# Optimization experiments

Measured on AMD Instinct MI355X. Metric: run time of the kernel, lower is better.

The kernel has to match this reference:

```python
import jax, jax.numpy as jnp
import numpy as np

NEG_INF = -9e15  # matches torch code's -9000000000000000.0
ALPHA = 0.1      # LeakyReLU negative slope


def setup_inputs() -> dict:
    key = jax.random.key(0)
    k1, k2, k3, k4 = jax.random.split(key, 4)
    N, D = 4096, 2048
    input_features = jax.random.normal(k1, (N, D), dtype=jnp.float32)
    adj_mat = jax.random.normal(k2, (N, N), dtype=jnp.float32)
    # parameters of GraphAttentionLayer(2048, 2048)
    W = jax.random.normal(k3, (D, D), dtype=jnp.float32) * 0.02
    a = jax.random.normal(k4, (2 * D, 1), dtype=jnp.float32) * 0.02
    return {"input_features": input_features, "adj_mat": adj_mat, "W": W, "a": a}


def reference(input_features, adj_mat, W, a):
    x = input_features  # [N, D]
    D = W.shape[1]
    # --- GNN.forward: cosine similarity adjacency ---
    dot = x @ x.T                                  # [N, N]
    lens = jnp.sqrt(jnp.sum(x * x, axis=1))        # [N]
    cos_sim = dot / (lens[:, None] * lens[None, :])
    new_adj = adj_mat * cos_sim                    # [N, N]
    # --- GraphAttentionLayer.forward ---
    h = x @ W                                      # [N, D]
    # concat trick: e_ij = leakyrelu(a1.h_i + a2.h_j), avoiding O(N^2*2D) tensor
    a1, a2 = a[:D, 0], a[D:, 0]
    s1 = h @ a1                                    # [N]
    s2 = h @ a2                                    # [N]
    e = jax.nn.leaky_relu(s1[:, None] + s2[None, :], ALPHA)  # [N, N]
    att_logits = jnp.where(new_adj > 0, e, NEG_INF)
    attention = jax.nn.softmax(att_logits, axis=1)  # dropout is identity at eval
    h_prime = attention @ h                        # [N, D]
    return jax.nn.elu(h_prime)                     # concat=True -> elu
```

## Files before the change

kernel.cpp:

```cpp
#include <hip/hip_runtime.h>
#include <hip/hip_bf16.h>
#include <cmath>

typedef unsigned short u16;
typedef unsigned char u8;
typedef unsigned int u32;
typedef __attribute__((ext_vector_type(8))) _Float16 f16x8;
typedef __attribute__((ext_vector_type(4))) float f32x4;

__device__ __forceinline__ float bf2f(u16 v) {
    union { u32 u; float f; } c; c.u = (u32)v << 16; return c.f;
}
__device__ __forceinline__ u16 f2bf(float f) {
    union { float f; u32 u; } c; c.f = f;
    u32 u = c.u;
    u += 0x7FFF + ((u >> 16) & 1);
    return (u16)(u >> 16);
}
__device__ __forceinline__ u16 f2h(float f) {
    _Float16 h = (_Float16)f; u16 r; __builtin_memcpy(&r, &h, 2); return r;
}
__device__ __forceinline__ float h2f(u16 b) {
    _Float16 h; __builtin_memcpy(&h, &b, 2); return (float)h;
}

__device__ __forceinline__ void gld_lds16(const void* g, void* l) {
    __builtin_amdgcn_global_load_lds(
        (const __attribute__((address_space(1))) void*)g,
        (__attribute__((address_space(3))) void*)l, 16, 0, 0);
}

__global__ __launch_bounds__(256) void sniff_kernel(const u16* __restrict__ x,
                                                    u32* __restrict__ flag) {
    const int t = threadIdx.x;
    int local = 0;
    for (int i = t; i < 4096; i += 256) {
        const int e = (x[i] >> 7) & 0xFF;
        if (e >= 110 && e <= 137) local++;
    }
#pragma unroll
    for (int o = 32; o > 0; o >>= 1) local += __shfl_down(local, o, 64);
    __shared__ int s[4];
    if ((t & 63) == 0) s[t >> 6] = local;
    __syncthreads();
    if (t == 0) {
        const int tot = s[0] + s[1] + s[2] + s[3];
        *flag = (tot >= 3200) ? 1u : 0u;
    }
}

__global__ __launch_bounds__(256) void prep_kernel(
    const void* __restrict__ xin, const void* __restrict__ Win,
    const void* __restrict__ ain,
    u16* __restrict__ xhi, u16* __restrict__ xlo,
    u16* __restrict__ WT, u16* __restrict__ aout,
    const u32* __restrict__ flag, int N, int D)
{
    __shared__ u16 tile[64][68];
    const bool isbf = (*flag != 0);
    const int b = blockIdx.x;
    const int t = threadIdx.x;

    if (b < 1024) {
        const long base = (long)b * 8192;
#pragma unroll
        for (int it = 0; it < 8; ++it) {
            const long i = base + (long)(it * 256 + t) * 4;
            float v[4];
            if (isbf) {
                ushort4 u = *(const ushort4*)((const u16*)xin + i);
                v[0] = bf2f(u.x); v[1] = bf2f(u.y); v[2] = bf2f(u.z); v[3] = bf2f(u.w);
            } else {
                float4 f = *(const float4*)((const float*)xin + i);
                v[0] = f.x; v[1] = f.y; v[2] = f.z; v[3] = f.w;
            }
            ushort4 hi, lo;
            u16* hp = &hi.x; u16* lp = &lo.x;
#pragma unroll
            for (int k = 0; k < 4; ++k) {
                _Float16 h = (_Float16)v[k];
                u16 hb; __builtin_memcpy(&hb, &h, 2);
                hp[k] = hb;
                lp[k] = f2h(v[k] - (float)h);
            }
            *(ushort4*)(xhi + i) = hi;
            *(ushort4*)(xlo + i) = lo;
        }
    } else if (b < 2048) {
        const int tt = b - 1024;
        const int bc = (tt & 31) * 64;
        const int br = (tt >> 5) * 64;
        const int lr = t >> 4;
        const int lc = (t & 15) * 4;
#pragma unroll
        for (int s = 0; s < 4; ++s) {
            const int r = lr + s * 16;
            float v[4];
            if (isbf) {
                ushort4 u = *(const ushort4*)((const u16*)Win + (size_t)(br + r) * D + bc + lc);
                v[0] = bf2f(u.x); v[1] = bf2f(u.y); v[2] = bf2f(u.z); v[3] = bf2f(u.w);
            } else {
                float4 f = *(const float4*)((const float*)Win + (size_t)(br + r) * D + bc + lc);
                v[0] = f.x; v[1] = f.y; v[2] = f.z; v[3] = f.w;
            }
            tile[r][lc + 0] = f2h(v[0]); tile[r][lc + 1] = f2h(v[1]);
            tile[r][lc + 2] = f2h(v[2]); tile[r][lc + 3] = f2h(v[3]);
        }
        __syncthreads();
#pragma unroll
        for (int s = 0; s < 4; ++s) {
            const int oc = lr + s * 16;
            ushort4 v;
            v.x = tile[lc + 0][oc]; v.y = tile[lc + 1][oc];
            v.z = tile[lc + 2][oc]; v.w = tile[lc + 3][oc];
            *(ushort4*)&WT[(size_t)(bc + oc) * D + br + lc] = v;
        }
    } else {
        for (int i = t; i < 2 * D; i += 256) {
            float v = isbf ? bf2f(((const u16*)ain)[i]) : ((const float*)ain)[i];
            aout[i] = f2h(v);
        }
    }
}

#define NMASK 528
#define MAXFIX 1024
#define MTAU 0.125f
__global__ __launch_bounds__(256, 2) void fused_mask_h(
    const u16* __restrict__ Xhi, const u16* __restrict__ Xlo, int ldx,
    u16* __restrict__ P, int N,
    const void* __restrict__ adj,
    const u16* __restrict__ WT, int D,
    u16* __restrict__ h,
    const u32* __restrict__ dflag)
{
    __shared__ alignas(16) u16 sm[2][128 * 64];

    const int tid = threadIdx.x;
    const int wave = tid >> 6, lane = tid & 63;
    const int wr = wave >> 1, wc = wave & 1;
    const int q = lane >> 4, mrow = lane & 15;
    const int srow8 = lane >> 3;
    const int gslot = (lane & 7) ^ srow8;

    const int bid = blockIdx.x;
    const bool isbf = (*dflag != 0);

    if (bid < NMASK) {
        const int idx = bid;
        int bm = (int)((__builtin_sqrtf(8.0f * idx + 1.0f) - 1.0f) * 0.5f);
        while ((bm + 1) * (bm + 2) / 2 <= idx) ++bm;
        while (bm * (bm + 1) / 2 > idx) --bm;
        const int bn = idx - bm * (bm + 1) / 2;

        const u16* Ab = Xhi + (size_t)bm * 128 * ldx;
        const u16* Bb = Xhi + (size_t)bn * 128 * ldx;

        f32x4 acc[4][4] = {};

        const int T = ldx >> 6;
        for (int t = 0; t < T; ++t) {
            const int kt = t * 64;
#pragma unroll
            for (int it = 0; it < 4; ++it) {
                const int c = wave * 4 + it;
                const int row = c * 8 + srow8;
                const size_t go = (size_t)row * ldx + kt + gslot * 8;
                gld_lds16(Ab + go, &sm[0][c * 512]);
                gld_lds16(Bb + go, &sm[1][c * 512]);
            }
            __syncthreads();

            f16x8 a[2][4], b[2][4];
#pragma unroll
            for (int ks = 0; ks < 2; ++ks)
#pragma unroll
                for (int i = 0; i < 4; ++i) {
                    const int ra = wr * 64 + i * 16 + mrow;
                    const int rb = wc * 64 + i * 16 + mrow;
                    const int sa = ((q + 4 * ks) ^ (mrow & 7)) * 8;
                    a[ks][i] = *(const f16x8*)&sm[0][ra * 64 + sa];
                    b[ks][i] = *(const f16x8*)&sm[1][rb * 64 + sa];
                }
#pragma unroll
            for (int i = 0; i < 4; ++i)
#pragma unroll
                for (int j = 0; j < 4; ++j) {
                    acc[i][j] = __builtin_amdgcn_mfma_f32_16x16x32_f16(
                        a[0][i], b[0][j], acc[i][j], 0, 0, 0);
                    acc[i][j] = __builtin_amdgcn_mfma_f32_16x16x32_f16(
                        a[1][i], b[1][j], acc[i][j], 0, 0, 0);
                }
            __syncthreads();
        }

        const u16* adjB = (const u16*)adj;
        const float* adjF = (const float*)adj;
        const float tau = isbf ? -1.0f : MTAU;

        u8* sgn = (u8*)sm;
        u32* list = (u32*)((u8*)sm + 24576);
        int* cntp = (int*)((u8*)sm + 28672);

        if (tid == 0) *cntp = 0;
#pragma unroll
        for (int i = 0; i < 4; ++i)
#pragma unroll
            for (int j = 0; j < 4; ++j)
#pragma unroll
                for (int r = 0; r < 4; ++r) {
                    const int rl = wr * 64 + i * 16 + q * 4 + r;
                    const int cl = wc * 64 + j * 16 + mrow;
                    const float v = acc[i][j][r];
                    sgn[rl * 132 + cl] = v > 0.f ? (u8)1
                                       : (v < 0.f ? (u8)2 : (u8)0);
                }
        __syncthreads();

#pragma unroll
        for (int i = 0; i < 4; ++i)
#pragma unroll
            for (int j = 0; j < 4; ++j)
#pragma unroll
                for (int r = 0; r < 4; ++r)
                    if (__builtin_fabsf(acc[i][j][r]) < tau) {
                        const int rl = wr * 64 + i * 16 + q * 4 + r;
                        const int cl = wc * 64 + j * 16 + mrow;
                        const int ix = atomicAdd(cntp, 1);
                        if (ix < MAXFIX) list[ix] = (u32)((rl << 8) | cl);
                    }
        __syncthreads();

        const int nfix = (*cntp < MAXFIX) ? *cntp : MAXFIX;
        for (int e = wave; e < nfix; e += 4) {
            const u32 pk = list[e];
            const int rl = (int)(pk >> 8), cl = (int)(pk & 255u);
            const u16* arh = Xhi + (size_t)(bm * 128 + rl) * ldx;
            const u16* arl = Xlo + (size_t)(bm * 128 + rl) * ldx;
            const u16* brh = Xhi + (size_t)(bn * 128 + cl) * ldx;
            const u16* brl = Xlo + (size_t)(bn * 128 + cl) * ldx;
            float ssum = 0.f;
#pragma unroll
            for (int kk = 0; kk < 4; ++kk) {
                const int k = kk * 512 + lane * 8;
                const f16x8 vah = *(const f16x8*)&arh[k];
                const f16x8 val2 = *(const f16x8*)&arl[k];
                const f16x8 vbh = *(const f16x8*)&brh[k];
                const f16x8 vbl = *(const f16x8*)&brl[k];
#pragma unroll
                for (int u = 0; u < 8; ++u)
                    ssum += ((float)vah[u] + (float)val2[u]) *
                            ((float)vbh[u] + (float)vbl[u]);
            }
#pragma unroll
            for (int o = 32; o > 0; o >>= 1) ssum += __shfl_xor(ssum, o, 64);
            if (lane == 0)
                sgn[rl * 132 + cl] = ssum > 0.f ? (u8)1
                                   : (ssum < 0.f ? (u8)2 : (u8)0);
        }
        __syncthreads();

        {
            const int c = tid & 127;
            const int r0 = tid >> 7;
#pragma unroll 4
            for (int s = 0; s < 64; ++s) {
                const int rr = r0 + 2 * s;
                const u8 s3 = sgn[rr * 132 + c];
                const size_t aidx = (size_t)(bm * 128 + rr) * N + bn * 128 + c;
                const float av = isbf ? bf2f(adjB[aidx]) : adjF[aidx];
                const bool f = (s3 == 1) ? (av > 0.f)
                             : (s3 == 2) ? (av < 0.f) : false;
                P[aidx] = f ? (u16)1 : (u16)0;
            }
        }

        if (bm != bn) {
            const int bl_ = tid & 63;
            const int a0 = tid >> 6;
#pragma unroll 4
            for (int s = 0; s < 32; ++s) {
                const int a = a0 + 4 * s;
#pragma unroll
                for (int hb = 0; hb < 2; ++hb) {
                    const int b = bl_ + 64 * hb;
                    const u8 s3 = sgn[b * 132 + a];
                    const size_t aidx = (size_t)(bn * 128 + a) * N + bm * 128 + b;
                    const float av = isbf ? bf2f(adjB[aidx]) : adjF[aidx];
                    const bool f = (s3 == 1) ? (av > 0.f)
                                 : (s3 == 2) ? (av < 0.f) : false;
                    P[aidx] = f ? (u16)1 : (u16)0;
                }
            }
        }
    } else {
        const int j = bid - NMASK;
        const int bn = j & 15;
        const int bm = j >> 4;

        const u16* Ab = Xhi + (size_t)bm * 128 * ldx;
        const u16* Bb = WT + (size_t)bn * 128 * D;

        f32x4 acc[4][4] = {};

        const int T = D >> 6;
        for (int t = 0; t < T; ++t) {
            const int kt = t * 64;
#pragma unroll
            for (int it = 0; it < 4; ++it) {
                const int c = wave * 4 + it;
                const int row = c * 8 + srow8;
                gld_lds16(Ab + (size_t)row * ldx + kt + gslot * 8,
                          &sm[0][c * 512]);
                gld_lds16(Bb + (size_t)row * D + kt + gslot * 8,
                          &sm[1][c * 512]);
            }
            __syncthreads();

            f16x8 a[2][4], b[2][4];
#pragma unroll
            for (int ks = 0; ks < 2; ++ks)
#pragma unroll
                for (int i = 0; i < 4; ++i) {
                    const int ra = wr * 64 + i * 16 + mrow;
                    const int rb = wc * 64 + i * 16 + mrow;
                    const int sa = ((q + 4 * ks) ^ (mrow & 7)) * 8;
                    a[ks][i] = *(const f16x8*)&sm[0][ra * 64 + sa];
                    b[ks][i] = *(const f16x8*)&sm[1][rb * 64 + sa];
                }
#pragma unroll
            for (int i = 0; i < 4; ++i)
#pragma unroll
                for (int jj = 0; jj < 4; ++jj) {
                    acc[i][jj] = __builtin_amdgcn_mfma_f32_16x16x32_f16(
                        a[0][i], b[0][jj], acc[i][jj], 0, 0, 0);
                    acc[i][jj] = __builtin_amdgcn_mfma_f32_16x16x32_f16(
                        a[1][i], b[1][jj], acc[i][jj], 0, 0, 0);
                }
            __syncthreads();
        }

        const int row0 = bm * 128 + wr * 64 + q * 4;
        const int col0 = bn * 128 + wc * 64 + mrow;
#pragma unroll
        for (int i = 0; i < 4; ++i)
#pragma unroll
            for (int jj = 0; jj < 4; ++jj)
#pragma unroll
                for (int r = 0; r < 4; ++r)
                    h[(size_t)(row0 + i * 16 + r) * D + col0 + jj * 16] =
                        f2h(acc[i][jj][r]);
    }
}

__global__ __launch_bounds__(256) void post1_kernel(
    const u16* __restrict__ h, const u16* __restrict__ a,
    float* __restrict__ s1, float* __restrict__ s2,
    u16* __restrict__ hT, int N, int D)
{
    __shared__ u16 tile[64][68];
    __shared__ float r1[4], r2[4];
    const int b = blockIdx.x;
    const int t = threadIdx.x;

    if (b < N) {
        const u16* hr = h + (size_t)b * D;
        const int k0 = t * 8;
        float acc1 = 0.f, acc2 = 0.f;
#pragma unroll
        for (int u = 0; u < 8; u += 4) {
            ushort4 hv  = *(const ushort4*)&hr[k0 + u];
            ushort4 a1v = *(const ushort4*)&a[k0 + u];
            ushort4 a2v = *(const ushort4*)&a[D + k0 + u];
            acc1 += h2f(hv.x) * h2f(a1v.x) + h2f(hv.y) * h2f(a1v.y)
                  + h2f(hv.z) * h2f(a1v.z) + h2f(hv.w) * h2f(a1v.w);
            acc2 += h2f(hv.x) * h2f(a2v.x) + h2f(hv.y) * h2f(a2v.y)
                  + h2f(hv.z) * h2f(a2v.z) + h2f(hv.w) * h2f(a2v.w);
        }
        const int lane = t & 63, wv = t >> 6;
#pragma unroll
        for (int o = 32; o > 0; o >>= 1) {
            acc1 += __shfl_down(acc1, o, 64);
            acc2 += __shfl_down(acc2, o, 64);
        }
        if (lane == 0) { r1[wv] = acc1; r2[wv] = acc2; }
        __syncthreads();
        if (t == 0) {
            s1[b] = r1[0] + r1[1] + r1[2] + r1[3];
            s2[b] = r2[0] + r2[1] + r2[2] + r2[3];
        }
    } else {
        const int tt = b - N;
        const int bc = (tt & 31) * 64;
        const int br = (tt >> 5) * 64;
        const int lr = t >> 4;
        const int lc = (t & 15) * 4;
#pragma unroll
        for (int s = 0; s < 4; ++s) {
            const int r = lr + s * 16;
            ushort4 v = *(const ushort4*)&h[(size_t)(br + r) * D + bc + lc];
            tile[r][lc + 0] = v.x; tile[r][lc + 1] = v.y;
            tile[r][lc + 2] = v.z; tile[r][lc + 3] = v.w;
        }
        __syncthreads();
#pragma unroll
        for (int s = 0; s < 4; ++s) {
            const int oc = lr + s * 16;
            ushort4 v;
            v.x = tile[lc + 0][oc]; v.y = tile[lc + 1][oc];
            v.z = tile[lc + 2][oc]; v.w = tile[lc + 3][oc];
            *(ushort4*)&hT[(size_t)(bc + oc) * N + br + lc] = v;
        }
    }
}

__global__ __launch_bounds__(256) void softmax_kernel(
    u16* __restrict__ P, const float* __restrict__ s1,
    const float* __restrict__ s2, int N)
{
    const int row = blockIdx.x;
    const int t = threadIdx.x;
    const int lane = t & 63, wv = t >> 6;
    u16* prow = P + (size_t)row * N;
    const float s1v = s1[row];

    float e[16];
#pragma unroll
    for (int it = 0; it < 16; ++it) {
        const int j = it * 256 + t;
        const u16 f = prow[j];
        float ev = s1v + s2[j];
        ev = ev >= 0.f ? ev : 0.1f * ev;
        e[it] = f ? ev : -9.0e15f;
    }
    float m = -3.4e38f;
#pragma unroll
    for (int it = 0; it < 16; ++it) m = fmaxf(m, e[it]);
#pragma unroll
    for (int o = 32; o > 0; o >>= 1) m = fmaxf(m, __shfl_xor(m, o, 64));
    __shared__ float red[8];
    if (lane == 0) red[wv] = m;
    __syncthreads();
    m = fmaxf(fmaxf(red[0], red[1]), fmaxf(red[2], red[3]));

    float sum = 0.f;
#pragma unroll
    for (int it = 0; it < 16; ++it) {
        e[it] = expf(fminf(e[it] - m, 0.0f));
        sum += e[it];
    }
#pragma unroll
    for (int o = 32; o > 0; o >>= 1) sum += __shfl_xor(sum, o, 64);
    if (lane == 0) red[4 + wv] = sum;
    __syncthreads();
    sum = red[4] + red[5] + red[6] + red[7];
    const float inv = 1.f / fmaxf(sum, 1e-30f);
#pragma unroll
    for (int it = 0; it < 16; ++it) {
        const int j = it * 256 + t;
        prow[j] = f2h(e[it] * inv);
    }
}

__global__ __launch_bounds__(256, 2) void gemm_elu(
    const u16* __restrict__ A, int lda,
    const u16* __restrict__ B, int ldb,
    u16* __restrict__ C, int ldc,
    int K, const u32* __restrict__ dflag)
{
    __shared__ alignas(16) u16 sm[2][128 * 64];

    const int tid = threadIdx.x;
    const int wave = tid >> 6, lane = tid & 63;
    const int wr = wave >> 1, wc = wave & 1;
    const int q = lane >> 4, mrow = lane & 15;
    const int srow8 = lane >> 3;
    const int gslot = (lane & 7) ^ srow8;

    const int bm = blockIdx.y;
    const int bn = blockIdx.x;

    const u16* Ab = A + (size_t)bm * 128 * lda;
    const u16* Bb = B + (size_t)bn * 128 * ldb;

    f32x4 acc[4][4] = {};

    const int T = K >> 6;
    for (int t = 0; t < T; ++t) {
        const int kt = t * 64;
#pragma unroll
        for (int it = 0; it < 4; ++it) {
            const int c = wave * 4 + it;
            const int row = c * 8 + srow8;
            gld_lds16(Ab + (size_t)row * lda + kt + gslot * 8, &sm[0][c * 512]);
            gld_lds16(Bb + (size_t)row * ldb + kt + gslot * 8, &sm[1][c * 512]);
        }
        __syncthreads();

        f16x8 a[2][4], b[2][4];
#pragma unroll
        for (int ks = 0; ks < 2; ++ks)
#pragma unroll
            for (int i = 0; i < 4; ++i) {
                const int ra = wr * 64 + i * 16 + mrow;
                const int rb = wc * 64 + i * 16 + mrow;
                const int sa = ((q + 4 * ks) ^ (mrow & 7)) * 8;
                a[ks][i] = *(const f16x8*)&sm[0][ra * 64 + sa];
                b[ks][i] = *(const f16x8*)&sm[1][rb * 64 + sa];
            }
#pragma unroll
        for (int i = 0; i < 4; ++i)
#pragma unroll
            for (int j = 0; j < 4; ++j) {
                acc[i][j] = __builtin_amdgcn_mfma_f32_16x16x32_f16(
                    a[0][i], b[0][j], acc[i][j], 0, 0, 0);
                acc[i][j] = __builtin_amdgcn_mfma_f32_16x16x32_f16(
                    a[1][i], b[1][j], acc[i][j], 0, 0, 0);
            }
        __syncthreads();
    }

    const bool isbf = (*dflag != 0);
    float* outF = (float*)C;
    const int row0 = bm * 128 + wr * 64 + q * 4;
    const int col0 = bn * 128 + wc * 64 + mrow;
#pragma unroll
    for (int i = 0; i < 4; ++i)
#pragma unroll
        for (int j = 0; j < 4; ++j)
#pragma unroll
            for (int r = 0; r < 4; ++r) {
                const int row = row0 + i * 16 + r;
                const int col = col0 + j * 16;
                const float v = acc[i][j][r];
                const float o = v > 0.0f ? v : expm1f(v);
                if (isbf) C[(size_t)row * ldc + col] = f2bf(o);
                else      outF[(size_t)row * ldc + col] = o;
            }
}

extern "C" void kernel_launch(void* const* d_in, const int* in_sizes, int n_in,
                              void* d_out, int out_size, void* d_ws, size_t ws_size,
                              hipStream_t stream)
{
    const void* x   = d_in[0];
    const void* adj = d_in[1];
    const void* W   = d_in[2];
    const void* a   = d_in[3];

    const int N = 4096, D = 2048;

    u16* xhi = (u16*)d_ws;
    u16* xlo = xhi + (size_t)N * D;
    u16* WT  = xlo + (size_t)N * D;
    u16* h   = WT  + (size_t)D * D;
    u16* P   = h   + (size_t)N * D;
    u16* af  = P   + (size_t)N * N;
    float* s1 = (float*)(af + 4096);
    float* s2 = s1 + N;
    u32* flag = (u32*)(s2 + N);

    sniff_kernel<<<1, 256, 0, stream>>>((const u16*)x, flag);
    prep_kernel<<<dim3(2049), 256, 0, stream>>>(x, W, a, xhi, xlo, WT, af,
                                                flag, N, D);
    fused_mask_h<<<dim3(1040), 256, 0, stream>>>(
        xhi, xlo, D, P, N, adj, WT, D, h, flag);
    post1_kernel<<<dim3(N + 2048), 256, 0, stream>>>(h, af, s1, s2, xlo, N, D);
    softmax_kernel<<<dim3(N), 256, 0, stream>>>(P, s1, s2, N);
    gemm_elu<<<dim3(D / 128, N / 128), 256, 0, stream>>>(
        P, N, xlo, N, (u16*)d_out, D, N, flag);
}
```

Baseline: 428.1 us.

## Precompute 2-bit adjacency sign map in prep kernel and vectorize mask writes

Adds 1024 blocks to the prep kernel that read the full adjacency matrix once, coalesced, and pack each element's sign into 2 bits. The mask epilogue in fused_mask_h then reads this compact map instead of strided fp32/bf16 adjacency values, and writes P as ushort4 vectors. The aim is to remove uncoalesced, transposed adjacency reads from the GEMM-tile epilogue. The cost is an extra full pass over adj plus a small sign buffer, and the 4-way byte gathers from sgn in the transposed path may cause LDS bank conflicts.

```diff
diff --git a/kernel.cpp b/kernel.cpp
--- a/kernel.cpp
+++ b/kernel.cpp
@@ -51,9 +51,10 @@
 
 __global__ __launch_bounds__(256) void prep_kernel(
     const void* __restrict__ xin, const void* __restrict__ Win,
-    const void* __restrict__ ain,
+    const void* __restrict__ ain, const void* __restrict__ adjin,
     u16* __restrict__ xhi, u16* __restrict__ xlo,
     u16* __restrict__ WT, u16* __restrict__ aout,
+    u8* __restrict__ asgn,
     const u32* __restrict__ flag, int N, int D)
 {
     __shared__ u16 tile[64][68];
@@ -115,10 +116,53 @@
             v.z = tile[lc + 2][oc]; v.w = tile[lc + 3][oc];
             *(ushort4*)&WT[(size_t)(bc + oc) * D + br + lc] = v;
         }
-    } else {
+    } else if (b == 2048) {
         for (int i = t; i < 2 * D; i += 256) {
             float v = isbf ? bf2f(((const u16*)ain)[i]) : ((const float*)ain)[i];
             aout[i] = f2h(v);
+        }
+    } else {
+        const long base = (long)(b - 2049) * 16384;
+#pragma unroll
+        for (int it = 0; it < 4; ++it) {
+            const long e0 = base + (long)(it * 256 + t) * 16;
+            u8 bytes[4];
+            if (isbf) {
+                const u16* ap = (const u16*)adjin + e0;
+#pragma unroll
+                for (int j = 0; j < 4; ++j) {
+                    ushort4 v = *(const ushort4*)(ap + j * 4);
+                    const u16 vv[4] = {v.x, v.y, v.z, v.w};
+                    u8 bb = 0;
+#pragma unroll
+                    for (int k = 0; k < 4; ++k) {
+                        const u16 m = (u16)(vv[k] & 0x7FFF);
+                        const u8 c = (m == 0) ? (u8)0
+                                   : ((vv[k] >> 15) ? (u8)2 : (u8)1);
+                        bb |= (u8)(c << (2 * k));
+                    }
+                    bytes[j] = bb;
+                }
+            } else {
+                const u32* ap = (const u32*)adjin + e0;
+#pragma unroll
+                for (int j = 0; j < 4; ++j) {
+                    uint4 v = *(const uint4*)(ap + j * 4);
+                    const u32 vv[4] = {v.x, v.y, v.z, v.w};
+                    u8 bb = 0;
+#pragma unroll
+                    for (int k = 0; k < 4; ++k) {
+                        const u32 m = vv[k] & 0x7FFFFFFFu;
+                        const u8 c = (m == 0) ? (u8)0
+                                   : ((vv[k] >> 31) ? (u8)2 : (u8)1);
+                        bb |= (u8)(c << (2 * k));
+                    }
+                    bytes[j] = bb;
+                }
+            }
+            uchar4 ov;
+            ov.x = bytes[0]; ov.y = bytes[1]; ov.z = bytes[2]; ov.w = bytes[3];
+            *(uchar4*)(asgn + (e0 >> 2)) = ov;
         }
     }
 }
@@ -129,7 +173,7 @@
 __global__ __launch_bounds__(256, 2) void fused_mask_h(
     const u16* __restrict__ Xhi, const u16* __restrict__ Xlo, int ldx,
     u16* __restrict__ P, int N,
-    const void* __restrict__ adj,
+    const u8* __restrict__ asgn,
     const u16* __restrict__ WT, int D,
     u16* __restrict__ h,
     const u32* __restrict__ dflag)
@@ -144,7 +188,6 @@
     const int gslot = (lane & 7) ^ srow8;
 
     const int bid = blockIdx.x;
-    const bool isbf = (*dflag != 0);
 
     if (bid < NMASK) {
         const int idx = bid;
@@ -194,8 +237,7 @@
             __syncthreads();
         }
 
-        const u16* adjB = (const u16*)adj;
-        const float* adjF = (const float*)adj;
+        const bool isbf = (*dflag != 0);
         const float tau = isbf ? -1.0f : MTAU;
 
         u8* sgn = (u8*)sm;
@@ -261,36 +303,39 @@
         __syncthreads();
 
         {
-            const int c = tid & 127;
-            const int r0 = tid >> 7;
-#pragma unroll 4
-            for (int s = 0; s < 64; ++s) {
-                const int rr = r0 + 2 * s;
-                const u8 s3 = sgn[rr * 132 + c];
-                const size_t aidx = (size_t)(bm * 128 + rr) * N + bn * 128 + c;
-                const float av = isbf ? bf2f(adjB[aidx]) : adjF[aidx];
-                const bool f = (s3 == 1) ? (av > 0.f)
-                             : (s3 == 2) ? (av < 0.f) : false;
-                P[aidx] = f ? (u16)1 : (u16)0;
+            const int c0 = (tid & 31) * 4;
+            const int r0 = tid >> 5;
+#pragma unroll
+            for (int s = 0; s < 16; ++s) {
+                const int rr = r0 + 8 * s;
+                const size_t aidx = (size_t)(bm * 128 + rr) * N + bn * 128 + c0;
+                const u8 ab = asgn[aidx >> 2];
+                const u32 sw = *(const u32*)&sgn[rr * 132 + c0];
+                ushort4 ov;
+                ov.x = ((sw         & 0xFF) & (u32)(ab        & 3)) ? (u16)1 : (u16)0;
+                ov.y = (((sw >>  8) & 0xFF) & (u32)((ab >> 2) & 3)) ? (u16)1 : (u16)0;
+                ov.z = (((sw >> 16) & 0xFF) & (u32)((ab >> 4) & 3)) ? (u16)1 : (u16)0;
+                ov.w = (((sw >> 24) & 0xFF) & (u32)((ab >> 6) & 3)) ? (u16)1 : (u16)0;
+                *(ushort4*)&P[aidx] = ov;
             }
         }
 
         if (bm != bn) {
-            const int bl_ = tid & 63;
-            const int a0 = tid >> 6;
-#pragma unroll 4
-            for (int s = 0; s < 32; ++s) {
-                const int a = a0 + 4 * s;
-#pragma unroll
-                for (int hb = 0; hb < 2; ++hb) {
-                    const int b = bl_ + 64 * hb;
-                    const u8 s3 = sgn[b * 132 + a];
-                    const size_t aidx = (size_t)(bn * 128 + a) * N + bm * 128 + b;
-                    const float av = isbf ? bf2f(adjB[aidx]) : adjF[aidx];
-                    const bool f = (s3 == 1) ? (av > 0.f)
-                                 : (s3 == 2) ? (av < 0.f) : false;
-                    P[aidx] = f ? (u16)1 : (u16)0;
-                }
+            const int b0 = (tid & 31) * 4;
+            const int a0 = tid >> 5;
+#pragma unroll
+            for (int s = 0; s < 16; ++s) {
+                const int a = a0 + 8 * s;
+                const size_t aidx = (size_t)(bn * 128 + a) * N + bm * 128 + b0;
+                const u8 ab = asgn[aidx >> 2];
+                ushort4 ov;
+                u16* op = &ov.x;
+#pragma unroll
+                for (int j = 0; j < 4; ++j) {
+                    const u8 s3 = sgn[(b0 + j) * 132 + a];
+                    op[j] = (u16)((s3 & ((ab >> (2 * j)) & 3)) ? 1 : 0);
+                }
+                *(ushort4*)&P[aidx] = ov;
             }
         }
     } else {
@@ -559,12 +604,13 @@
     float* s1 = (float*)(af + 4096);
     float* s2 = s1 + N;
     u32* flag = (u32*)(s2 + N);
+    u8* asgn = (u8*)(flag + 16);
 
     sniff_kernel<<<1, 256, 0, stream>>>((const u16*)x, flag);
-    prep_kernel<<<dim3(2049), 256, 0, stream>>>(x, W, a, xhi, xlo, WT, af,
-                                                flag, N, D);
+    prep_kernel<<<dim3(3073), 256, 0, stream>>>(x, W, a, adj, xhi, xlo, WT, af,
+                                                asgn, flag, N, D);
     fused_mask_h<<<dim3(1040), 256, 0, stream>>>(
-        xhi, xlo, D, P, N, adj, WT, D, h, flag);
+        xhi, xlo, D, P, N, asgn, WT, D, h, flag);
     post1_kernel<<<dim3(N + 2048), 256, 0, stream>>>(h, af, s1, s2, xlo, N, D);
     softmax_kernel<<<dim3(N), 256, 0, stream>>>(P, s1, s2, N);
     gemm_elu<<<dim3(D / 128, N / 128), 256, 0, stream>>>(
```

After: 392.9 us. -8.2%, faster.
